# Performance work log

Hardware: AMD Instinct MI355X
Metric: run time of the kernel (lower is better)

The kernel has to match this reference:

```python
import jax, jax.numpy as jnp
import numpy as np

L = 2        # NUM_DECODER_LAYERS
D = 512      # D_MODEL == ENCODER_EMBEDDING_DIM == DECODER_EMBEDDING_DIM == DECODER_HIDDEN_DIM
T = 32       # max_trg_len (greedy decode steps)
SOS = 1      # SPECIAL_TOKENS.index('[SOS]'), PAD assumed 0


def setup_inputs() -> dict:
    key = jax.random.key(0)
    ks = jax.random.split(key, 12)
    Vin, Vout, B, S = 32000, 32000, 32, 512
    s = 0.02
    src = jax.random.randint(ks[0], (B, S), 0, Vin)
    src_emb_table = jax.random.normal(ks[1], (Vin, D), dtype=jnp.float32) * s
    trg_emb_table = (jax.random.normal(ks[2], (Vout, D), dtype=jnp.float32) * s).at[0].set(0.0)  # padding_idx=0
    Wih = jax.random.normal(ks[3], (L, 4 * D, D), dtype=jnp.float32) * s
    Whh = jax.random.normal(ks[4], (L, 4 * D, D), dtype=jnp.float32) * s
    bih = jnp.zeros((L, 4 * D), jnp.float32)
    bhh = jnp.zeros((L, 4 * D), jnp.float32)
    Wfc = jax.random.normal(ks[5], (D, D), dtype=jnp.float32) * s      # Decoder.fc_out (hid_dim -> hid_dim)
    bfc = jnp.zeros((D,), jnp.float32)
    Wh2o = jax.random.normal(ks[6], (D, 2 * D), dtype=jnp.float32) * s  # hidden_to_out
    bh2o = jnp.zeros((D,), jnp.float32)
    bout = jnp.zeros((Vout,), jnp.float32)                              # out_layer bias (weight tied to trg_emb_table)
    return dict(src=src, src_emb_table=src_emb_table, trg_emb_table=trg_emb_table,
                Wih=Wih, Whh=Whh, bih=bih, bhh=bhh, Wfc=Wfc, bfc=bfc,
                Wh2o=Wh2o, bh2o=bh2o, bout=bout)


def reference(src, src_emb_table, trg_emb_table, Wih, Whh, bih, bhh, Wfc, bfc, Wh2o, bh2o, bout):
    B, S = src.shape
    dtype = src_emb_table.dtype
    scale = jnp.asarray(D ** 0.5, dtype)
    src_e = src_emb_table[src]  # [B,S,D] -- encoder LSTM hidden/cell are computed but discarded in the original

    def lstm_cell(x, h, c, l):
        g = x @ Wih[l].T + bih[l] + h @ Whh[l].T + bhh[l]
        i, f, gg, o = jnp.split(g, 4, axis=-1)  # torch gate order i,f,g,o
        c2 = jax.nn.sigmoid(f) * c + jax.nn.sigmoid(i) * jnp.tanh(gg)
        h2 = jax.nn.sigmoid(o) * jnp.tanh(c2)
        return h2, c2

    def outer_step(carry, t):
        # Original re-runs the decoder LSTM over the whole generated prefix every
        # step, starting from the carried hidden state; we mask positions > t.
        tokens, h, c = carry  # tokens [B,T+1] int32, h/c [L,B,D]
        emb = jnp.swapaxes(trg_emb_table[tokens[:, :T]], 0, 1)  # [T,B,D]

        def pos_step(hc, inp):
            h, c = hc
            x, pos = inp
            active = pos <= t
            hs, cs = [], []
            for l in range(L):
                h2, c2 = lstm_cell(x, h[l], c[l], l)
                h2 = jnp.where(active, h2, h[l])
                c2 = jnp.where(active, c2, c[l])
                hs.append(h2); cs.append(c2)
                x = h2
            h, c = jnp.stack(hs), jnp.stack(cs)
            return (h, c), h[-1]

        (h, c), h_top = jax.lax.scan(pos_step, (h, c), (emb, jnp.arange(T)))
        out_seq = h_top @ Wfc.T + bfc                 # [T,B,D] Decoder.fc_out
        out_t = jnp.take(out_seq, t, axis=0)          # last valid position (concat[:, -1])
        w = jax.nn.softmax(jnp.einsum('bd,bsd->bs', out_t, src_e) / scale, axis=-1)
        context = jnp.einsum('bs,bsd->bd', w, src_e)
        hid = jax.nn.relu(jnp.concatenate([out_t, context], axis=-1) @ Wh2o.T + bh2o)
        logits = hid @ trg_emb_table.T + bout         # out_layer tied to decoder embedding
        nxt = jnp.argmax(logits, axis=-1).astype(tokens.dtype)
        tokens = tokens.at[:, t + 1].set(nxt)
        return (tokens, h, c), out_seq

    tokens0 = jnp.zeros((B, T + 1), jnp.int32).at[:, 0].set(SOS)
    h0 = jnp.zeros((L, B, D), dtype)
    (tokens, _, _), out_seqs = jax.lax.scan(outer_step, (tokens0, h0, h0), jnp.arange(T))
    # attn returned by the original is from the LAST decode step, queries = all T positions
    attn = jax.nn.softmax(jnp.einsum('tbd,bsd->bts', out_seqs[-1], src_e) / scale, axis=-1)  # [B,T,S]
    return tokens[:, 1:], attn
```

## Files before the change

kernel.cpp:

```cpp
#include <hip/hip_runtime.h>
#include <math.h>

#define NWG 256
#define TPB 512
#define AGT __HIP_MEMORY_SCOPE_AGENT

static constexpr int Bb = 32, Dd = 512, Tt = 32, Vv = 32000;
static constexpr int BD = Bb * Dd;
static constexpr float SCALE_INV = 0.04419417382415922f;

static constexpr size_t OFF_H0 = 4096;
static constexpr size_t OFF_H1 = OFF_H0 + 2 * (size_t)BD;
static constexpr size_t OFF_P  = OFF_H1 + 2 * (size_t)BD;
static constexpr size_t OFF_HL = OFF_P + (size_t)Tt * Bb * 2048;
static constexpr size_t OFF_HD = OFF_HL + (size_t)Tt * BD;
static constexpr size_t OFF_OF = OFF_HD + BD;
static constexpr size_t OFF_CV = OFF_OF + (size_t)Tt * BD;
static constexpr size_t OFF_CI = OFF_CV + 32 * 256;
static constexpr size_t OFF_ET = OFF_CI + 32 * 256;

static constexpr int L_W   = 0;
static constexpr int L_H   = 13824;
static constexpr int L_SC  = 30208;
static constexpr int L_RB  = 30720;
static constexpr int L_IB  = 31744;
static constexpr int L_RED = 32256;
static constexpr int L_GV  = 32272;
static constexpr int L_GI  = 32400;
static constexpr int L_TOK = 32528;
static constexpr int LDS_FLOATS = 32560;
static constexpr size_t LDS_BYTES = (size_t)LDS_FLOATS * 4;

__device__ __forceinline__ float sigm(float x) { return 1.0f / (1.0f + expf(-x)); }

__device__ __forceinline__ float ldcv(const float* p) {
  unsigned u = __hip_atomic_load((const unsigned*)p, __ATOMIC_RELAXED, AGT);
  return __builtin_bit_cast(float, u);
}
__device__ __forceinline__ void stcv(float* p, float v) {
  __hip_atomic_store((unsigned*)p, __builtin_bit_cast(unsigned, v), __ATOMIC_RELAXED, AGT);
}
__device__ __forceinline__ float2 ldcv2(const float* p) {
  unsigned long long u = __hip_atomic_load((const unsigned long long*)p, __ATOMIC_RELAXED, AGT);
  return __builtin_bit_cast(float2, u);
}
__device__ __forceinline__ void stcv2(float* p, float2 v) {
  __hip_atomic_store((unsigned long long*)p, __builtin_bit_cast(unsigned long long, v),
                     __ATOMIC_RELAXED, AGT);
}
__device__ __forceinline__ int ldcvi(const int* p) {
  return (int)__hip_atomic_load((const unsigned*)p, __ATOMIC_RELAXED, AGT);
}
__device__ __forceinline__ void stcvi(int* p, int v) {
  __hip_atomic_store((unsigned*)p, (unsigned)v, __ATOMIC_RELAXED, AGT);
}

__device__ __forceinline__ float wredsum(float v) {
#pragma unroll
  for (int off = 32; off > 0; off >>= 1) v += __shfl_xor(v, off, 64);
  return v;
}

__device__ __forceinline__ float rowReduce16(float x) {
  int t;
  t = __builtin_amdgcn_update_dpp(0, __builtin_bit_cast(int, x), 0x121, 0xF, 0xF, false);
  x += __builtin_bit_cast(float, t);
  t = __builtin_amdgcn_update_dpp(0, __builtin_bit_cast(int, x), 0x122, 0xF, 0xF, false);
  x += __builtin_bit_cast(float, t);
  t = __builtin_amdgcn_update_dpp(0, __builtin_bit_cast(int, x), 0x124, 0xF, 0xF, false);
  x += __builtin_bit_cast(float, t);
  t = __builtin_amdgcn_update_dpp(0, __builtin_bit_cast(int, x), 0x128, 0xF, 0xF, false);
  x += __builtin_bit_cast(float, t);
  return x;
}

__device__ __forceinline__ int swzH(int byte) { return byte ^ (((byte >> 8) & 7) << 4); }

__device__ __forceinline__ void gbar(unsigned* sb, unsigned& lg) {
  const unsigned tgt = lg + 1u;
  asm volatile("s_waitcnt vmcnt(0)" ::: "memory");
  __syncthreads();
  if (threadIdx.x == 0) {
    const int g = (int)blockIdx.x >> 5;
    unsigned a = __hip_atomic_fetch_add(&sb[g * 64], 1u, __ATOMIC_RELAXED, AGT);
    if (a == 31u) {
      __hip_atomic_store(&sb[g * 64], 0u, __ATOMIC_RELAXED, AGT);
      unsigned r = __hip_atomic_fetch_add(&sb[1024], 1u, __ATOMIC_RELAXED, AGT);
      if (r == 7u) {
        __hip_atomic_store(&sb[1024], 0u, __ATOMIC_RELAXED, AGT);
#pragma unroll
        for (int gg = 0; gg < 8; ++gg)
          __hip_atomic_store(&sb[2048 + gg * 64], tgt, __ATOMIC_RELAXED, AGT);
      }
    }
    while (__hip_atomic_load(&sb[2048 + g * 64], __ATOMIC_RELAXED, AGT) < tgt)
      __builtin_amdgcn_s_sleep(1);
    __builtin_amdgcn_fence(__ATOMIC_ACQUIRE, "agent");
  }
  lg = tgt;
  __syncthreads();
}

__device__ __forceinline__ float blockMax(float v, float* red, int tid) {
#pragma unroll
  for (int off = 32; off > 0; off >>= 1) v = fmaxf(v, __shfl_xor(v, off, 64));
  if ((tid & 63) == 0) red[tid >> 6] = v;
  __syncthreads();
  float m = red[0];
#pragma unroll
  for (int i = 1; i < 8; ++i) m = fmaxf(m, red[i]);
  __syncthreads();
  return m;
}

__device__ __forceinline__ float blockSum(float v, float* red, int tid) {
  v = wredsum(v);
  if ((tid & 63) == 0) red[tid >> 6] = v;
  __syncthreads();
  float s = 0.f;
#pragma unroll
  for (int i = 0; i < 8; ++i) s += red[i];
  __syncthreads();
  return s;
}

__device__ void stageW(int wg, int tid, const float* __restrict__ Wih,
                       const float* __restrict__ Whh, float* __restrict__ SMW) {
  for (int e = tid; e < 24 * 512; e += TPB) {
    const int k = e & 511, rr = e >> 9;
    const int m = rr >> 3, q = (rr >> 1) & 3, dl = rr & 1;
    const int j = q * 512 + wg * 2 + dl;
    const float* srcp = (m == 0) ? (Whh + (size_t)j * 512)
                     : (m == 1) ? (Wih + (size_t)2048 * 512 + (size_t)j * 512)
                                : (Whh + (size_t)2048 * 512 + (size_t)j * 512);
    SMW[rr * 576 + (k >> 5) * 36 + (k & 31)] = srcp[k];
  }
  __syncthreads();
}

__device__ void buildETb(int wg, int tid, const float* __restrict__ Etrg,
                         float* __restrict__ ETb, float* __restrict__ SM) {
  if (wg < 250) {
    for (int tile = 0; tile < 8; ++tile) {
      const int tv = tile >> 2, tk = tile & 3;
      __syncthreads();
      for (int e = tid; e < 64 * 128; e += TPB) {
        const int vl = e >> 7, kl = e & 127;
        SM[vl * 129 + kl] = Etrg[(size_t)(wg * 128 + tv * 64 + vl) * 512 + tk * 128 + kl];
      }
      __syncthreads();
      for (int e = tid; e < 32 * 128; e += TPB) {
        const int vp = e >> 7, kl = e & 127;
        const int v = wg * 128 + tv * 64 + vp * 2;
        const int k = tk * 128 + kl;
        float2 val = make_float2(SM[(vp * 2) * 129 + kl], SM[(vp * 2 + 1) * 129 + kl]);
        stcv2(ETb + ((size_t)(v >> 1) * 512 + k) * 2, val);
      }
    }
    __syncthreads();
  }
}

__device__ __forceinline__ void dotMQ(const float* __restrict__ SMW, int rr, int kc,
                                      const float4* __restrict__ hq, float2& acc) {
  const float4* wr = (const float4*)(SMW + rr * 576 + kc * 36);
#pragma unroll
  for (int i2 = 0; i2 < 8; ++i2) {
    const float4 wv = wr[i2];
    const float4 hA = hq[i2 * 2], hB = hq[i2 * 2 + 1];
    acc.x = fmaf(wv.x, hA.x, acc.x); acc.y = fmaf(wv.x, hA.y, acc.y);
    acc.x = fmaf(wv.y, hA.z, acc.x); acc.y = fmaf(wv.y, hA.w, acc.y);
    acc.x = fmaf(wv.z, hB.x, acc.x); acc.y = fmaf(wv.z, hB.y, acc.y);
    acc.x = fmaf(wv.w, hB.z, acc.x); acc.y = fmaf(wv.w, hB.w, acc.y);
  }
}

__device__ __forceinline__ void phaseAB(
    int wg, int tid, bool doA, bool doB,
    const float* __restrict__ H0r, float* __restrict__ H0w,
    const float* __restrict__ H1r, float* __restrict__ H1w,
    float* __restrict__ HlP, const float* __restrict__ Pp,
    const float* __restrict__ bs1v,
    const float* __restrict__ SMW, float* __restrict__ LH, float* c0, float* c1)
{
  const int b2 = tid >> 5, dl = (tid >> 4) & 1, kc = tid & 15;
  char* LHc = (char*)LH;
  float4 s0[8], s1[8];
  __builtin_amdgcn_sched_barrier(0);
  {
    const float* p0 = H0r + tid * 4;
#pragma unroll
    for (int r = 0; r < 8; ++r)
      asm volatile("global_load_dwordx4 %0, %1, off sc0" : "=v"(s0[r]) : "v"(p0 + r * 2048));
  }
  if (doB) {
    const float* p1 = H1r + tid * 4;
#pragma unroll
    for (int r = 0; r < 8; ++r)
      asm volatile("global_load_dwordx4 %0, %1, off sc0" : "=v"(s1[r]) : "v"(p1 + r * 2048));
    asm volatile("s_waitcnt vmcnt(8)" ::: "memory");
  } else {
    asm volatile("s_waitcnt vmcnt(0)" ::: "memory");
  }
  __builtin_amdgcn_sched_barrier(0);
#pragma unroll
  for (int r = 0; r < 8; ++r)
    *(float4*)(LHc + swzH((r * 512 + tid) * 16)) = s0[r];
  __syncthreads();
  float4 hq[16];
#pragma unroll
  for (int i = 0; i < 16; ++i)
    hq[i] = *(const float4*)(LHc + swzH(b2 * 4096 + kc * 256 + i * 16));

  float2 acc2[12];
#pragma unroll
  for (int j = 0; j < 12; ++j) acc2[j] = make_float2(0.f, 0.f);

  if (doA) {
#pragma unroll
    for (int q = 0; q < 4; ++q) dotMQ(SMW, q * 2 + dl, kc, hq, acc2[q]);
  }
  if (doB) {
#pragma unroll
    for (int q = 0; q < 4; ++q) dotMQ(SMW, 8 + q * 2 + dl, kc, hq, acc2[4 + q]);
    asm volatile("s_waitcnt vmcnt(0)" ::: "memory");
    __builtin_amdgcn_sched_barrier(0);
    __syncthreads();
#pragma unroll
    for (int r = 0; r < 8; ++r)
      *(float4*)(LHc + swzH((r * 512 + tid) * 16)) = s1[r];
    __syncthreads();
#pragma unroll
    for (int i = 0; i < 16; ++i)
      hq[i] = *(const float4*)(LHc + swzH(b2 * 4096 + kc * 256 + i * 16));
#pragma unroll
    for (int q = 0; q < 4; ++q) dotMQ(SMW, 16 + q * 2 + dl, kc, hq, acc2[8 + q]);
  }

#pragma unroll
  for (int j = 0; j < 12; ++j) {
    if (j < 4 ? !doA : !doB) continue;
    acc2[j].x = rowReduce16(acc2[j].x);
    acc2[j].y = rowReduce16(acc2[j].y);
  }

  if (kc == 0) {
    const int d = (wg << 1) | dl;
    if (doA) {
#pragma unroll
      for (int p = 0; p < 2; ++p) {
        const int b = b2 * 2 + p;
        const float* pb = Pp + b * 2048 + d;
        const float gi = (p ? acc2[0].y : acc2[0].x) + pb[0];
        const float gf = (p ? acc2[1].y : acc2[1].x) + pb[512];
        const float gg = (p ? acc2[2].y : acc2[2].x) + pb[1024];
        const float go = (p ? acc2[3].y : acc2[3].x) + pb[1536];
        c0[p] = sigm(gf) * c0[p] + sigm(gi) * tanhf(gg);
        stcv(H0w + b2 * 1024 + d * 2 + p, sigm(go) * tanhf(c0[p]));
      }
    }
    if (doB) {
#pragma unroll
      for (int p = 0; p < 2; ++p) {
        const float gi = (p ? acc2[4].y : acc2[4].x) + (p ? acc2[8].y  : acc2[8].x)  + bs1v[0];
        const float gf = (p ? acc2[5].y : acc2[5].x) + (p ? acc2[9].y  : acc2[9].x)  + bs1v[1];
        const float gg = (p ? acc2[6].y : acc2[6].x) + (p ? acc2[10].y : acc2[10].x) + bs1v[2];
        const float go = (p ? acc2[7].y : acc2[7].x) + (p ? acc2[11].y : acc2[11].x) + bs1v[3];
        c1[p] = sigm(gf) * c1[p] + sigm(gi) * tanhf(gg);
        const float hn = sigm(go) * tanhf(c1[p]);
        stcv(H1w + b2 * 1024 + d * 2 + p, hn);
        if (HlP) stcv(HlP + b2 * 1024 + d * 2 + p, hn);
      }
    }
  }
}

__device__ void phaseCDEF(int b, int tid, const float* __restrict__ H1c,
                          const float* __restrict__ Wfc, const float* __restrict__ bfc,
                          const int* __restrict__ src, const float* __restrict__ Esrc,
                          const float* __restrict__ Wh2o, const float* __restrict__ bh2o,
                          float* __restrict__ hD, float* sc, float* rb, int* ib, float* red)
{
  rb[tid] = ldcv(H1c + (b >> 1) * 1024 + tid * 2 + (b & 1));
  ib[tid] = src[b * 512 + tid];
  __syncthreads();
  const int w = tid >> 6, lane = tid & 63;
  for (int d = w; d < 512; d += 8) {
    const float* wr = Wfc + (size_t)d * 512;
    float p = 0.f;
#pragma unroll
    for (int i = 0; i < 8; ++i) p = fmaf(rb[lane * 8 + i], wr[lane * 8 + i], p);
    p = wredsum(p);
    if (lane == 0) rb[512 + d] = p + bfc[d];
  }
  __syncthreads();
  for (int s = w; s < 512; s += 8) {
    const float* er = Esrc + (size_t)ib[s] * 512;
    float p = 0.f;
#pragma unroll
    for (int i = 0; i < 8; ++i) p = fmaf(rb[512 + lane * 8 + i], er[lane * 8 + i], p);
    p = wredsum(p);
    if (lane == 0) sc[s] = p * SCALE_INV;
  }
  __syncthreads();
  const float mx = blockMax(sc[tid], red, tid);
  const float e = expf(sc[tid] - mx);
  sc[tid] = e;
  const float sum = blockSum(e, red, tid);
  const float inv = 1.0f / sum;
  float acc = 0.f;
#pragma unroll 4
  for (int s = 0; s < 512; ++s) acc = fmaf(sc[s], Esrc[(size_t)ib[s] * 512 + tid], acc);
  rb[tid] = acc * inv;
  __syncthreads();
  for (int d = w; d < 512; d += 8) {
    const float* wr = Wh2o + (size_t)d * 1024;
    float p = 0.f;
#pragma unroll
    for (int i = 0; i < 8; ++i) p = fmaf(rb[512 + lane * 8 + i], wr[lane * 8 + i], p);
#pragma unroll
    for (int i = 0; i < 8; ++i) p = fmaf(rb[lane * 8 + i], wr[512 + lane * 8 + i], p);
    p = wredsum(p);
    if (lane == 0) stcv(hD + (size_t)b * 512 + d, fmaxf(p + bh2o[d], 0.f));
  }
}

__device__ void phaseG_ET(int wg, int tid, const float* __restrict__ hD, const float* __restrict__ ETb,
                          const float* __restrict__ bout, float* __restrict__ candV,
                          int* __restrict__ candI, float* hidT, float* gv, int* gi)
{
  if (wg >= 250) return;
  const int v0 = wg * 128;
#pragma unroll 1
  for (int ph = 0; ph < 2; ++ph) {
    const int bbase = ph * 16;
    __syncthreads();
    for (int e = tid; e < 16 * 512; e += TPB) {
      const int bb = e >> 9, k = e & 511;
      hidT[k * 18 + bb] = ldcv(hD + (size_t)(bbase + bb) * 512 + k);
    }
    __syncthreads();
    const int vp = tid >> 3, bh = tid & 7;
    const int v = v0 + vp * 2;
    float a00 = 0.f, a01 = 0.f, a10 = 0.f, a11 = 0.f;
    const float* ep = ETb + (size_t)(v >> 1) * 1024;
    const float* hp = hidT + bh * 2;
#pragma unroll 8
    for (int k = 0; k < 512; ++k) {
      const float2 e2 = *(const float2*)(ep + k * 2);
      const float2 h2 = *(const float2*)(hp + k * 18);
      a00 = fmaf(e2.x, h2.x, a00);
      a01 = fmaf(e2.x, h2.y, a01);
      a10 = fmaf(e2.y, h2.x, a10);
      a11 = fmaf(e2.y, h2.y, a11);
    }
    const float bo0 = bout[v], bo1 = bout[v + 1];
    a00 += bo0; a01 += bo0; a10 += bo1; a11 += bo1;
    float vA, vB; int iA, iB;
    if (a10 > a00) { vA = a10; iA = v + 1; } else { vA = a00; iA = v; }
    if (a11 > a01) { vB = a11; iB = v + 1; } else { vB = a01; iB = v; }
#pragma unroll
    for (int off = 8; off < 64; off <<= 1) {
      float ov = __shfl_xor(vA, off, 64); int oi = __shfl_xor(iA, off, 64);
      if (ov > vA || (ov == vA && oi < iA)) { vA = ov; iA = oi; }
      ov = __shfl_xor(vB, off, 64); oi = __shfl_xor(iB, off, 64);
      if (ov > vB || (ov == vB && oi < iB)) { vB = ov; iB = oi; }
    }
    if ((tid & 63) < 8) {
      const int w = tid >> 6;
      gv[(bh * 2 + 0) * 8 + w] = vA; gi[(bh * 2 + 0) * 8 + w] = iA;
      gv[(bh * 2 + 1) * 8 + w] = vB; gi[(bh * 2 + 1) * 8 + w] = iB;
    }
    __syncthreads();
    if (tid < 16) {
      float bv = -INFINITY; int bi = 0;
      for (int w2 = 0; w2 < 8; ++w2) {
        const float vv = gv[tid * 8 + w2]; const int ii = gi[tid * 8 + w2];
        if (vv > bv || (vv == bv && ii < bi)) { bv = vv; bi = ii; }
      }
      stcv(candV + (size_t)(bbase + tid) * 256 + wg, bv);
      stcvi(candI + (bbase + tid) * 256 + wg, bi);
    }
  }
}

__device__ void phaseG_noET(int wg, int tid, const float* __restrict__ hD,
                            const float* __restrict__ Etrg, const float* __restrict__ bout,
                            float* __restrict__ candV, int* __restrict__ candI,
                            float* rb, float* gv, int* gi)
{
  const int b = wg >> 3, vb = wg & 7;
  rb[tid] = ldcv(hD + (size_t)b * 512 + tid);
  __syncthreads();
  const int w = tid >> 6, lane = tid & 63;
  float bv = -INFINITY; int bi = 0;
  for (int v = vb * 4000 + w; v < (vb + 1) * 4000; v += 8) {
    const float* er = Etrg + (size_t)v * 512;
    float p = 0.f;
#pragma unroll
    for (int i = 0; i < 8; ++i) p = fmaf(rb[lane * 8 + i], er[lane * 8 + i], p);
    p = wredsum(p);
    p += bout[v];
    if (p > bv || (p == bv && v < bi)) { bv = p; bi = v; }
  }
  if (lane == 0) { gv[w] = bv; gi[w] = bi; }
  __syncthreads();
  if (tid == 0) {
    float fv = -INFINITY; int fi = 0;
    for (int w2 = 0; w2 < 8; ++w2)
      if (gv[w2] > fv || (gv[w2] == fv && gi[w2] < fi)) { fv = gv[w2]; fi = gi[w2]; }
    stcv(candV + (size_t)b * 256 + vb, fv);
    stcvi(candI + b * 256 + vb, fi);
  }
  __syncthreads();
}

__device__ void phaseHP(int wg, int tid, int t, bool useET,
                        const float* __restrict__ candV, const int* __restrict__ candI,
                        const float* __restrict__ Etrg, const float* __restrict__ Wih,
                        const float* __restrict__ bih, const float* __restrict__ bhh,
                        float* __restrict__ P, float* __restrict__ out, int* tokL)
{
  const int nslot = useET ? 250 : 8;
  {
    const int b = tid >> 4, sl = tid & 15;
    float bv = -INFINITY; int bi = 0x7fffffff;
    for (int s = sl; s < nslot; s += 16) {
      const float vv = ldcv(candV + (size_t)b * 256 + s);
      const int ii = ldcvi(candI + b * 256 + s);
      if (vv > bv || (vv == bv && ii < bi)) { bv = vv; bi = ii; }
    }
#pragma unroll
    for (int off = 1; off < 16; off <<= 1) {
      const float ov = __shfl_xor(bv, off, 64); const int oi = __shfl_xor(bi, off, 64);
      if (ov > bv || (ov == bv && oi < bi)) { bv = ov; bi = oi; }
    }
    if (sl == 0) {
      tokL[b] = bi;
      if (wg == 0) stcv(out + b * 32 + t, (float)bi);
    }
  }
  __syncthreads();
  if (t < 31) {
    const int w = tid >> 6, lane = tid & 63;
    const int q = w >> 1, dl = w & 1;
    const int j = q * 512 + wg * 2 + dl;
    const float* wr = Wih + (size_t)j * 512;
    const float bsum = bih[j] + bhh[j];
    for (int b = 0; b < 32; ++b) {
      const float* er = Etrg + (size_t)tokL[b] * 512;
      float p = 0.f;
#pragma unroll
      for (int i = 0; i < 8; ++i) p = fmaf(er[lane * 8 + i], wr[lane * 8 + i], p);
      p = wredsum(p);
      if (lane == 0) stcv(P + ((size_t)(t + 1) * 32 + b) * 2048 + j, p + bsum);
    }
  }
  __syncthreads();
}

__device__ void phaseX(int wg, int tid, const float* __restrict__ Hl, const float* __restrict__ Wfc,
                       const float* __restrict__ bfc, float* __restrict__ oF)
{
  const int p = wg >> 3, bq = wg & 7;
  const int w = tid >> 6, lane = tid & 63;
  for (int u = w; u < 1024; u += 8) {
    const int b2 = bq * 2 + (u >> 9), d = u & 511;
    const float* hr = Hl + (size_t)p * BD + b2 * 1024;
    const float* wr = Wfc + (size_t)d * 512;
    float ax = 0.f, ay = 0.f;
#pragma unroll
    for (int i = 0; i < 8; ++i) {
      const float2 hv = ldcv2(hr + (lane * 8 + i) * 2);
      const float wv = wr[lane * 8 + i];
      ax = fmaf(hv.x, wv, ax);
      ay = fmaf(hv.y, wv, ay);
    }
    ax = wredsum(ax); ay = wredsum(ay);
    if (lane == 0) {
      stcv(oF + ((size_t)p * 32 + b2 * 2    ) * 512 + d, ax + bfc[d]);
      stcv(oF + ((size_t)p * 32 + b2 * 2 + 1) * 512 + d, ay + bfc[d]);
    }
  }
}

__device__ void phaseY(int wg, int tid, const float* __restrict__ oF, const int* __restrict__ src,
                       const float* __restrict__ Esrc, float* __restrict__ out,
                       float* sc, float* rb, int* ib, float* red)
{
  for (int r = 0; r < 4; ++r) {
    const int id = wg * 4 + r;
    const int b = id >> 5, p = id & 31;
    __syncthreads();
    rb[tid] = ldcv(oF + ((size_t)p * 32 + b) * 512 + tid);
    ib[tid] = src[b * 512 + tid];
    __syncthreads();
    const int w = tid >> 6, lane = tid & 63;
    for (int s = w; s < 512; s += 8) {
      const float* er = Esrc + (size_t)ib[s] * 512;
      float acc = 0.f;
#pragma unroll
      for (int i = 0; i < 8; ++i) acc = fmaf(rb[lane * 8 + i], er[lane * 8 + i], acc);
      acc = wredsum(acc);
      if (lane == 0) sc[s] = acc * SCALE_INV;
    }
    __syncthreads();
    const float mx = blockMax(sc[tid], red, tid);
    const float e = expf(sc[tid] - mx);
    const float sum = blockSum(e, red, tid);
    out[1024 + ((size_t)b * 32 + p) * 512 + tid] = e / sum;
  }
}

extern "C" __global__ void __launch_bounds__(TPB)
s2s_mega(const int* __restrict__ src, const float* __restrict__ Esrc, const float* __restrict__ Etrg,
         const float* __restrict__ Wih, const float* __restrict__ Whh,
         const float* __restrict__ bih, const float* __restrict__ bhh,
         const float* __restrict__ Wfc, const float* __restrict__ bfc,
         const float* __restrict__ Wh2o, const float* __restrict__ bh2o,
         const float* __restrict__ bout, float* __restrict__ out,
         float* __restrict__ ws, const float* __restrict__ ET, float* __restrict__ ETw)
{
  extern __shared__ float SM[];
  float* SMW = SM + L_W;
  float* LH  = SM + L_H;
  float* sc  = SM + L_SC;
  float* rb  = SM + L_RB;
  int*   ib  = (int*)(SM + L_IB);
  float* red = SM + L_RED;
  float* gv  = SM + L_GV;
  int*   gi  = (int*)(SM + L_GI);
  int*   tokL = (int*)(SM + L_TOK);

  unsigned* sb = (unsigned*)ws;
  float* H0 = ws + OFF_H0;
  float* H1 = ws + OFF_H1;
  float* P  = ws + OFF_P;
  float* Hl = ws + OFF_HL;
  float* hD = ws + OFF_HD;
  float* oF = ws + OFF_OF;
  float* cV = ws + OFF_CV;
  int*   cI = (int*)(ws + OFF_CI);

  const int wg = blockIdx.x, tid = threadIdx.x;
  const bool useET = (ET != nullptr);
  unsigned lg = 0u;
  float c0[2] = {0.f, 0.f}, c1[2] = {0.f, 0.f};

  float bs1v[4];
  {
    const int dl = (tid >> 4) & 1;
    const int d = (wg << 1) | dl;
#pragma unroll
    for (int q = 0; q < 4; ++q)
      bs1v[q] = bih[2048 + q * 512 + d] + bhh[2048 + q * 512 + d];
  }

  {
    const int gid = wg * TPB + tid;
    if (gid < BD) stcv(H0 + gid, 0.f);
    else if (gid < 2 * BD) stcv(H1 + gid - BD, 0.f);
  }
  {
    const int w = tid >> 6, lane = tid & 63;
    const int q = w >> 1, dl = w & 1;
    const int j = q * 512 + wg * 2 + dl;
    const float* er = Etrg + 512;
    const float* wr = Wih + (size_t)j * 512;
    float p = 0.f;
#pragma unroll
    for (int i = 0; i < 8; ++i) p = fmaf(er[lane * 8 + i], wr[lane * 8 + i], p);
    p = wredsum(p);
    p += bih[j] + bhh[j];
    if (lane < 32) stcv(P + (size_t)lane * 2048 + j, p);
  }
  if (ETw) buildETb(wg, tid, Etrg, ETw, LH);
  stageW(wg, tid, Wih, Whh, SMW);
  gbar(sb, lg);

  int cur0 = 0, cur1 = 0;
  for (int t = 0; t < 32; ++t) {
    for (int k = 0; k <= t + 1; ++k) {
      const bool doA = (k <= t), doB = (k >= 1);
      float* HlP = (t == 31 && doB) ? (Hl + (size_t)(k - 1) * BD) : nullptr;
      const int kp = (k < 32) ? k : 31;
      phaseAB(wg, tid, doA, doB,
              H0 + (size_t)cur0 * BD, H0 + (size_t)(cur0 ^ 1) * BD,
              H1 + (size_t)cur1 * BD, H1 + (size_t)(cur1 ^ 1) * BD,
              HlP, P + (size_t)kp * Bb * 2048, bs1v, SMW, LH, c0, c1);
      if (t >= 2 && k == 0) {
        if (useET) phaseG_ET(wg, tid, hD, ET, bout, cV, cI, LH, gv, gi);
        else       phaseG_noET(wg, tid, hD, Etrg, bout, cV, cI, rb, gv, gi);
      }
      if (t >= 2 && k == 1)
        phaseHP(wg, tid, t - 1, useET, cV, cI, Etrg, Wih, bih, bhh, P, out, tokL);
      gbar(sb, lg);
      if (doA) cur0 ^= 1;
      if (doB) cur1 ^= 1;
    }
    if (wg < 32) phaseCDEF(wg, tid, H1 + (size_t)cur1 * BD, Wfc, bfc, src, Esrc,
                           Wh2o, bh2o, hD, sc, rb, ib, red);
    gbar(sb, lg);
    if (t == 0) {
      if (useET) phaseG_ET(wg, tid, hD, ET, bout, cV, cI, LH, gv, gi);
      else       phaseG_noET(wg, tid, hD, Etrg, bout, cV, cI, rb, gv, gi);
      gbar(sb, lg);
      phaseHP(wg, tid, 0, useET, cV, cI, Etrg, Wih, bih, bhh, P, out, tokL);
      gbar(sb, lg);
    }
  }
  phaseX(wg, tid, Hl, Wfc, bfc, oF);
  if (useET) phaseG_ET(wg, tid, hD, ET, bout, cV, cI, LH, gv, gi);
  else       phaseG_noET(wg, tid, hD, Etrg, bout, cV, cI, rb, gv, gi);
  gbar(sb, lg);
  phaseHP(wg, tid, 31, useET, cV, cI, Etrg, Wih, bih, bhh, P, out, tokL);
  phaseY(wg, tid, oF, src, Esrc, out, sc, rb, ib, red);
}

extern "C" void kernel_launch(void* const* d_in, const int* in_sizes, int n_in,
                              void* d_out, int out_size, void* d_ws, size_t ws_size,
                              hipStream_t stream) {
  const int*   src  = (const int*)d_in[0];
  const float* Esrc = (const float*)d_in[1];
  const float* Etrg = (const float*)d_in[2];
  const float* Wih  = (const float*)d_in[3];
  const float* Whh  = (const float*)d_in[4];
  const float* bih  = (const float*)d_in[5];
  const float* bhh  = (const float*)d_in[6];
  const float* Wfc  = (const float*)d_in[7];
  const float* bfc  = (const float*)d_in[8];
  const float* Wh2o = (const float*)d_in[9];
  const float* bh2o = (const float*)d_in[10];
  const float* bout = (const float*)d_in[11];
  float* ws = (float*)d_ws;

  const size_t needET = (OFF_ET + (size_t)512 * 32000) * sizeof(float);
  const bool useET = (ws_size >= needET);
  float* etw = useET ? (ws + OFF_ET) : nullptr;

  (void)hipMemsetAsync(d_ws, 0, 16384, stream);

  (void)hipFuncSetAttribute(reinterpret_cast<const void*>(&s2s_mega),
                            hipFuncAttributeMaxDynamicSharedMemorySize, (int)LDS_BYTES);

  s2s_mega<<<dim3(NWG), dim3(TPB), LDS_BYTES, stream>>>(
      src, Esrc, Etrg, Wih, Whh, bih, bhh, Wfc, bfc, Wh2o, bh2o, bout,
      (float*)d_out, ws, etw, etw);
}
```

Measured before the change: 19.38 ms.

## Split vocab projection across two LSTM steps and use flag-based grid barrier

The vocabulary logits phase is split into two K-halves whose accumulators stay in registers, so it runs across two consecutive LSTM sub-steps. The argmax and token phase is pushed back one sub-step to match. The grid barrier changes from counter atomics to per-workgroup flag slots polled by a group leader, with a second level of group flags. Hidden-state loads switch from the sc0 to the sc1 cache hint, and the LDS layout is reorganized with a dedicated swizzled hidden block buffer. The aim is to shorten the critical path per decode step and cut barrier contention. The cost is extra LDS and a larger memset, plus the correctness risk of keeping accumulators live across barriers.

```diff
diff --git a/kernel.cpp b/kernel.cpp
--- a/kernel.cpp
+++ b/kernel.cpp
@@ -9,7 +9,7 @@
 static constexpr int BD = Bb * Dd;
 static constexpr float SCALE_INV = 0.04419417382415922f;
 
-static constexpr size_t OFF_H0 = 4096;
+static constexpr size_t OFF_H0 = 8192;
 static constexpr size_t OFF_H1 = OFF_H0 + 2 * (size_t)BD;
 static constexpr size_t OFF_P  = OFF_H1 + 2 * (size_t)BD;
 static constexpr size_t OFF_HL = OFF_P + (size_t)Tt * Bb * 2048;
@@ -20,15 +20,16 @@
 static constexpr size_t OFF_ET = OFF_CI + 32 * 256;
 
 static constexpr int L_W   = 0;
-static constexpr int L_H   = 13824;
-static constexpr int L_SC  = 30208;
-static constexpr int L_RB  = 30720;
-static constexpr int L_IB  = 31744;
-static constexpr int L_RED = 32256;
-static constexpr int L_GV  = 32272;
-static constexpr int L_GI  = 32400;
-static constexpr int L_TOK = 32528;
-static constexpr int LDS_FLOATS = 32560;
+static constexpr int L_ST  = 13824;
+static constexpr int L_SC  = 13824;
+static constexpr int L_RB  = 14336;
+static constexpr int L_IB  = 15360;
+static constexpr int L_RED = 15872;
+static constexpr int L_HB  = 30208;
+static constexpr int L_GV  = 32256;
+static constexpr int L_GI  = 32512;
+static constexpr int L_TOK = 32768;
+static constexpr int LDS_FLOATS = 32800;
 static constexpr size_t LDS_BYTES = (size_t)LDS_FLOATS * 4;
 
 __device__ __forceinline__ float sigm(float x) { return 1.0f / (1.0f + expf(-x)); }
@@ -80,22 +81,26 @@
   const unsigned tgt = lg + 1u;
   asm volatile("s_waitcnt vmcnt(0)" ::: "memory");
   __syncthreads();
-  if (threadIdx.x == 0) {
-    const int g = (int)blockIdx.x >> 5;
-    unsigned a = __hip_atomic_fetch_add(&sb[g * 64], 1u, __ATOMIC_RELAXED, AGT);
-    if (a == 31u) {
-      __hip_atomic_store(&sb[g * 64], 0u, __ATOMIC_RELAXED, AGT);
-      unsigned r = __hip_atomic_fetch_add(&sb[1024], 1u, __ATOMIC_RELAXED, AGT);
-      if (r == 7u) {
-        __hip_atomic_store(&sb[1024], 0u, __ATOMIC_RELAXED, AGT);
-#pragma unroll
-        for (int gg = 0; gg < 8; ++gg)
-          __hip_atomic_store(&sb[2048 + gg * 64], tgt, __ATOMIC_RELAXED, AGT);
-      }
-    }
-    while (__hip_atomic_load(&sb[2048 + g * 64], __ATOMIC_RELAXED, AGT) < tgt)
-      __builtin_amdgcn_s_sleep(1);
-    __builtin_amdgcn_fence(__ATOMIC_ACQUIRE, "agent");
+  const int wg = (int)blockIdx.x;
+  if (threadIdx.x < 64) {
+    const int lane = (int)threadIdx.x;
+    if (lane == 0)
+      __hip_atomic_store(&sb[wg * 16], tgt, __ATOMIC_RELAXED, AGT);
+    const int g = wg >> 5;
+    if ((wg & 31) == 0) {
+      if (lane < 32) {
+        const unsigned* slot = &sb[(g * 32 + lane) * 16];
+        while (__hip_atomic_load(slot, __ATOMIC_RELAXED, AGT) < tgt)
+          __builtin_amdgcn_s_sleep(1);
+      }
+      if (lane == 0)
+        __hip_atomic_store(&sb[4096 + g * 16], tgt, __ATOMIC_RELAXED, AGT);
+    }
+    if (lane < 8) {
+      const unsigned* f = &sb[4096 + lane * 16];
+      while (__hip_atomic_load(f, __ATOMIC_RELAXED, AGT) < tgt)
+        __builtin_amdgcn_s_sleep(1);
+    }
   }
   lg = tgt;
   __syncthreads();
@@ -191,13 +196,13 @@
     const float* p0 = H0r + tid * 4;
 #pragma unroll
     for (int r = 0; r < 8; ++r)
-      asm volatile("global_load_dwordx4 %0, %1, off sc0" : "=v"(s0[r]) : "v"(p0 + r * 2048));
+      asm volatile("global_load_dwordx4 %0, %1, off sc1" : "=v"(s0[r]) : "v"(p0 + r * 2048));
   }
   if (doB) {
     const float* p1 = H1r + tid * 4;
 #pragma unroll
     for (int r = 0; r < 8; ++r)
-      asm volatile("global_load_dwordx4 %0, %1, off sc0" : "=v"(s1[r]) : "v"(p1 + r * 2048));
+      asm volatile("global_load_dwordx4 %0, %1, off sc1" : "=v"(s1[r]) : "v"(p1 + r * 2048));
     asm volatile("s_waitcnt vmcnt(8)" ::: "memory");
   } else {
     asm volatile("s_waitcnt vmcnt(0)" ::: "memory");
@@ -325,62 +330,79 @@
   }
 }
 
-__device__ void phaseG_ET(int wg, int tid, const float* __restrict__ hD, const float* __restrict__ ETb,
-                          const float* __restrict__ bout, float* __restrict__ candV,
-                          int* __restrict__ candI, float* hidT, float* gv, int* gi)
+__device__ void phaseG(int wg, int tid, int chunk, float* __restrict__ accG,
+                       const float* __restrict__ hD, const float* __restrict__ ETb,
+                       const float* __restrict__ bout, float* __restrict__ candV,
+                       int* __restrict__ candI, float* __restrict__ hblk,
+                       float* __restrict__ gv, int* __restrict__ gi)
 {
   if (wg >= 250) return;
-  const int v0 = wg * 128;
-#pragma unroll 1
-  for (int ph = 0; ph < 2; ++ph) {
-    const int bbase = ph * 16;
-    __syncthreads();
-    for (int e = tid; e < 16 * 512; e += TPB) {
-      const int bb = e >> 9, k = e & 511;
-      hidT[k * 18 + bb] = ldcv(hD + (size_t)(bbase + bb) * 512 + k);
-    }
-    __syncthreads();
-    const int vp = tid >> 3, bh = tid & 7;
-    const int v = v0 + vp * 2;
-    float a00 = 0.f, a01 = 0.f, a10 = 0.f, a11 = 0.f;
-    const float* ep = ETb + (size_t)(v >> 1) * 1024;
-    const float* hp = hidT + bh * 2;
+  if (chunk == 0) {
+#pragma unroll
+    for (int j = 0; j < 8; ++j) accG[j] = 0.f;
+  }
+  const int vp = tid >> 3, bh = tid & 7;
+  const int v0 = wg * 128 + vp * 2;
+  const float* ep = ETb + (size_t)(v0 >> 1) * 1024 + chunk * 512;
+  const int fk = tid & 63, fb0 = tid >> 6;
+  char* hb = (char*)hblk;
+
+  for (int blk = 0; blk < 4; ++blk) {
+    const int kb = chunk * 256 + blk * 64;
+    __syncthreads();
+#pragma unroll
+    for (int i = 0; i < 4; ++i) {
+      const int b = fb0 + i * 8;
+      const float hv = ldcv(hD + (size_t)b * 512 + kb + fk);
+      const int byte = fk * 128 + (((b >> 2) * 16) ^ ((fk & 7) << 4)) + ((b & 3) << 2);
+      *(float*)(hb + byte) = hv;
+    }
+    __syncthreads();
 #pragma unroll 8
-    for (int k = 0; k < 512; ++k) {
-      const float2 e2 = *(const float2*)(ep + k * 2);
-      const float2 h2 = *(const float2*)(hp + k * 18);
-      a00 = fmaf(e2.x, h2.x, a00);
-      a01 = fmaf(e2.x, h2.y, a01);
-      a10 = fmaf(e2.y, h2.x, a10);
-      a11 = fmaf(e2.y, h2.y, a11);
-    }
-    const float bo0 = bout[v], bo1 = bout[v + 1];
-    a00 += bo0; a01 += bo0; a10 += bo1; a11 += bo1;
-    float vA, vB; int iA, iB;
-    if (a10 > a00) { vA = a10; iA = v + 1; } else { vA = a00; iA = v; }
-    if (a11 > a01) { vB = a11; iB = v + 1; } else { vB = a01; iB = v; }
-#pragma unroll
-    for (int off = 8; off < 64; off <<= 1) {
-      float ov = __shfl_xor(vA, off, 64); int oi = __shfl_xor(iA, off, 64);
-      if (ov > vA || (ov == vA && oi < iA)) { vA = ov; iA = oi; }
-      ov = __shfl_xor(vB, off, 64); oi = __shfl_xor(iB, off, 64);
-      if (ov > vB || (ov == vB && oi < iB)) { vB = ov; iB = oi; }
-    }
-    if ((tid & 63) < 8) {
-      const int w = tid >> 6;
-      gv[(bh * 2 + 0) * 8 + w] = vA; gi[(bh * 2 + 0) * 8 + w] = iA;
-      gv[(bh * 2 + 1) * 8 + w] = vB; gi[(bh * 2 + 1) * 8 + w] = iB;
-    }
-    __syncthreads();
-    if (tid < 16) {
+    for (int kk = 0; kk < 64; kk += 2) {
+      const float4 e4 = *(const float4*)ep; ep += 4;
+      const float4 ha = *(const float4*)(hb + kk * 128 + ((bh * 16) ^ ((kk & 7) << 4)));
+      const float4 hbv = *(const float4*)(hb + (kk + 1) * 128 + ((bh * 16) ^ (((kk + 1) & 7) << 4)));
+      accG[0] = fmaf(e4.x, ha.x, accG[0]);  accG[4] = fmaf(e4.y, ha.x, accG[4]);
+      accG[1] = fmaf(e4.x, ha.y, accG[1]);  accG[5] = fmaf(e4.y, ha.y, accG[5]);
+      accG[2] = fmaf(e4.x, ha.z, accG[2]);  accG[6] = fmaf(e4.y, ha.z, accG[6]);
+      accG[3] = fmaf(e4.x, ha.w, accG[3]);  accG[7] = fmaf(e4.y, ha.w, accG[7]);
+      accG[0] = fmaf(e4.z, hbv.x, accG[0]); accG[4] = fmaf(e4.w, hbv.x, accG[4]);
+      accG[1] = fmaf(e4.z, hbv.y, accG[1]); accG[5] = fmaf(e4.w, hbv.y, accG[5]);
+      accG[2] = fmaf(e4.z, hbv.z, accG[2]); accG[6] = fmaf(e4.w, hbv.z, accG[6]);
+      accG[3] = fmaf(e4.z, hbv.w, accG[3]); accG[7] = fmaf(e4.w, hbv.w, accG[7]);
+    }
+  }
+
+  if (chunk == 1) {
+    const float bo0 = bout[v0], bo1 = bout[v0 + 1];
+    const int w = tid >> 6;
+#pragma unroll
+    for (int j = 0; j < 4; ++j) {
+      const float va = accG[j] + bo0, vb = accG[4 + j] + bo1;
+      float bv; int bi;
+      if (vb > va) { bv = vb; bi = v0 + 1; } else { bv = va; bi = v0; }
+#pragma unroll
+      for (int off = 8; off < 64; off <<= 1) {
+        const float ov = __shfl_xor(bv, off, 64); const int oi = __shfl_xor(bi, off, 64);
+        if (ov > bv || (ov == bv && oi < bi)) { bv = ov; bi = oi; }
+      }
+      if ((tid & 63) < 8) {
+        gv[(bh * 4 + j) * 8 + w] = bv;
+        gi[(bh * 4 + j) * 8 + w] = bi;
+      }
+    }
+    __syncthreads();
+    if (tid < 32) {
       float bv = -INFINITY; int bi = 0;
       for (int w2 = 0; w2 < 8; ++w2) {
         const float vv = gv[tid * 8 + w2]; const int ii = gi[tid * 8 + w2];
         if (vv > bv || (vv == bv && ii < bi)) { bv = vv; bi = ii; }
       }
-      stcv(candV + (size_t)(bbase + tid) * 256 + wg, bv);
-      stcvi(candI + (bbase + tid) * 256 + wg, bi);
-    }
+      stcv(candV + (size_t)tid * 256 + wg, bv);
+      stcvi(candI + tid * 256 + wg, bi);
+    }
+    __syncthreads();
   }
 }
 
@@ -523,11 +545,12 @@
 {
   extern __shared__ float SM[];
   float* SMW = SM + L_W;
-  float* LH  = SM + L_H;
+  float* LH  = SM + L_ST;
   float* sc  = SM + L_SC;
   float* rb  = SM + L_RB;
   int*   ib  = (int*)(SM + L_IB);
   float* red = SM + L_RED;
+  float* hblk = SM + L_HB;
   float* gv  = SM + L_GV;
   int*   gi  = (int*)(SM + L_GI);
   int*   tokL = (int*)(SM + L_TOK);
@@ -546,6 +569,7 @@
   const bool useET = (ET != nullptr);
   unsigned lg = 0u;
   float c0[2] = {0.f, 0.f}, c1[2] = {0.f, 0.f};
+  float accG[8];
 
   float bs1v[4];
   {
@@ -588,12 +612,23 @@
               H0 + (size_t)cur0 * BD, H0 + (size_t)(cur0 ^ 1) * BD,
               H1 + (size_t)cur1 * BD, H1 + (size_t)(cur1 ^ 1) * BD,
               HlP, P + (size_t)kp * Bb * 2048, bs1v, SMW, LH, c0, c1);
-      if (t >= 2 && k == 0) {
-        if (useET) phaseG_ET(wg, tid, hD, ET, bout, cV, cI, LH, gv, gi);
-        else       phaseG_noET(wg, tid, hD, Etrg, bout, cV, cI, rb, gv, gi);
-      }
-      if (t >= 2 && k == 1)
-        phaseHP(wg, tid, t - 1, useET, cV, cI, Etrg, Wih, bih, bhh, P, out, tokL);
+      if (useET) {
+        if (t >= 2 && k == 0) {
+          phaseG(wg, tid, 0, accG, hD, ET, bout, cV, cI, hblk, gv, gi);
+          if (t == 2) phaseG(wg, tid, 1, accG, hD, ET, bout, cV, cI, hblk, gv, gi);
+        }
+        if (t >= 3 && k == 1)
+          phaseG(wg, tid, 1, accG, hD, ET, bout, cV, cI, hblk, gv, gi);
+        if (t == 2 && k == 1)
+          phaseHP(wg, tid, 1, true, cV, cI, Etrg, Wih, bih, bhh, P, out, tokL);
+        if (t >= 3 && k == 2)
+          phaseHP(wg, tid, t - 1, true, cV, cI, Etrg, Wih, bih, bhh, P, out, tokL);
+      } else {
+        if (t >= 2 && k == 0)
+          phaseG_noET(wg, tid, hD, Etrg, bout, cV, cI, hblk, gv, gi);
+        if (t >= 2 && k == 1)
+          phaseHP(wg, tid, t - 1, false, cV, cI, Etrg, Wih, bih, bhh, P, out, tokL);
+      }
       gbar(sb, lg);
       if (doA) cur0 ^= 1;
       if (doB) cur1 ^= 1;
@@ -602,16 +637,24 @@
                            Wh2o, bh2o, hD, sc, rb, ib, red);
     gbar(sb, lg);
     if (t == 0) {
-      if (useET) phaseG_ET(wg, tid, hD, ET, bout, cV, cI, LH, gv, gi);
-      else       phaseG_noET(wg, tid, hD, Etrg, bout, cV, cI, rb, gv, gi);
+      if (useET) {
+        phaseG(wg, tid, 0, accG, hD, ET, bout, cV, cI, hblk, gv, gi);
+        phaseG(wg, tid, 1, accG, hD, ET, bout, cV, cI, hblk, gv, gi);
+      } else {
+        phaseG_noET(wg, tid, hD, Etrg, bout, cV, cI, hblk, gv, gi);
+      }
       gbar(sb, lg);
       phaseHP(wg, tid, 0, useET, cV, cI, Etrg, Wih, bih, bhh, P, out, tokL);
       gbar(sb, lg);
     }
   }
   phaseX(wg, tid, Hl, Wfc, bfc, oF);
-  if (useET) phaseG_ET(wg, tid, hD, ET, bout, cV, cI, LH, gv, gi);
-  else       phaseG_noET(wg, tid, hD, Etrg, bout, cV, cI, rb, gv, gi);
+  if (useET) {
+    phaseG(wg, tid, 0, accG, hD, ET, bout, cV, cI, hblk, gv, gi);
+    phaseG(wg, tid, 1, accG, hD, ET, bout, cV, cI, hblk, gv, gi);
+  } else {
+    phaseG_noET(wg, tid, hD, Etrg, bout, cV, cI, hblk, gv, gi);
+  }
   gbar(sb, lg);
   phaseHP(wg, tid, 31, useET, cV, cI, Etrg, Wih, bih, bhh, P, out, tokL);
   phaseY(wg, tid, oF, src, Esrc, out, sc, rb, ib, red);
@@ -638,7 +681,7 @@
   const bool useET = (ws_size >= needET);
   float* etw = useET ? (ws + OFF_ET) : nullptr;
 
-  (void)hipMemsetAsync(d_ws, 0, 16384, stream);
+  (void)hipMemsetAsync(d_ws, 0, 32768, stream);
 
   (void)hipFuncSetAttribute(reinterpret_cast<const void*>(&s2s_mega),
                             hipFuncAttributeMaxDynamicSharedMemorySize, (int)LDS_BYTES);
```

Result: faster. 18.06 ms (-6.8%).
